# Optimization experiments

Measured on AMD Instinct MI355X. Metric: run time of the kernel, lower is better.

The kernel has to match this reference:

```python
import jax, jax.numpy as jnp
import numpy as np

BETA = 0.25  # commitment-loss weight


def setup_inputs() -> dict:
    key = jax.random.key(0)
    k1, k2 = jax.random.split(key)
    # x: [B, H, W, D] so that x.reshape(-1, D) groups per-pixel latent vectors
    x = jax.random.normal(k1, (32, 64, 64, 64), dtype=jnp.float32)
    # codebook: [D, K] as in the torch module (embedding_dim, num_embeddings)
    embedding = jax.random.normal(k2, (64, 1024), dtype=jnp.float32)
    return {"x": x, "embedding": embedding}


def reference(x, embedding):
    D, K = embedding.shape
    flat = x.reshape(-1, D)  # [N, D]
    # pairwise squared distances: ||z||^2 + ||e||^2 - 2 z.e  -> [N, K]
    distances = (
        jnp.sum(flat * flat, axis=1, keepdims=True)
        + jnp.sum(embedding * embedding, axis=0)
        - 2.0 * (flat @ embedding)
    )
    encoding_indices = jnp.argmin(distances, axis=1)  # [N]
    encodings = jax.nn.one_hot(encoding_indices, K, dtype=x.dtype)  # [N, K]
    # gather codewords (same math as encodings @ embedding.T, but O(N*D))
    quantized = jnp.take(embedding, encoding_indices, axis=1).T.reshape(x.shape)
    e_latent_loss = jnp.mean((jax.lax.stop_gradient(quantized) - x) ** 2)
    loss = BETA * e_latent_loss
    # straight-through estimator
    quantized_st = x + jax.lax.stop_gradient(quantized - x)
    avg_probs = jnp.mean(encodings, axis=0)
    perplexity = jnp.exp(-jnp.sum(avg_probs * jnp.log(avg_probs + 1e-10)))
    return quantized_st, loss, perplexity, encodings, encoding_indices
```

## Files before the change

### kernel.cpp

```cpp
#include <hip/hip_runtime.h>
#include <math.h>

#define NPIX    131072
#define DDIM    64
#define KCODE   1024
#define BETA    0.25f
#define EPS2    4e-3f
#define FIXCAP  2048
#define TAILROW 130944

#define Q_OFF    0
#define LOSS_OFF 8388608
#define PERP_OFF 8388609
#define ENC_OFF  8388610
#define IDX_OFF  142606338

#define TAIL_F     134086656
#define EHS_F      (TAIL_F + 2)
#define ELS_F      (TAIL_F + 32770)
#define FIXLIST_I  (TAIL_F + 65540)
#define FIXDELTA_F (TAIL_F + 69638)
#define FIXCOUNT_I (TAIL_F + 71688)


typedef _Float16 half8 __attribute__((ext_vector_type(8)));
typedef float    f32x4 __attribute__((ext_vector_type(4)));
typedef __attribute__((address_space(3))) void       lds_void_t;
typedef __attribute__((address_space(1))) const void g_void_t;

__global__ void vq_prep(const float* __restrict__ emb, float* __restrict__ embT,
                        _Float16* __restrict__ ehs, _Float16* __restrict__ els,
                        float* __restrict__ norms) {
    int b = blockIdx.x;
    if (b < 256) {
        int i = b * 256 + threadIdx.x;
        int d = i >> 10;
        int k = i & 1023;
        float v = emb[i];
        embT[k * DDIM + d] = v;
        _Float16 h = (_Float16)v;
        _Float16 l = (_Float16)(v - (float)h);
        int panel = k >> 6, codeP = k & 63;
        int sw = (d >> 3) ^ (k & 7);
        int fi = panel * 4096 + codeP * 64 + sw * 8 + (d & 7);
        ehs[fi] = h;
        els[fi] = l;
    } else {
        int k = (b - 256) * 256 + threadIdx.x;
        float s = 0.f;
        #pragma unroll 8
        for (int d = 0; d < DDIM; ++d) {
            float v = emb[d * KCODE + k];
            s = fmaf(v, v, s);
        }
        norms[k] = s;
    }
}

__global__ __launch_bounds__(256) void vq_fused(
        const float* __restrict__ x, const _Float16* __restrict__ ehs,
        const _Float16* __restrict__ els, const float* __restrict__ norms,
        const float* __restrict__ embT, float* __restrict__ idxf,
        float* __restrict__ q, float* __restrict__ enc,
        int* __restrict__ hist, float* __restrict__ lossp,
        int* __restrict__ fixlist, int* __restrict__ fixcount) {
    __shared__ __align__(16) char lds_raw[17152];

    const int tid  = threadIdx.x;
    const int role = blockIdx.x & 1;
    const int rid  = blockIdx.x >> 1;

    if (role == 1) {
        const long long NSEG = 33521663LL;
        f32x4* basep = (f32x4*)(enc + 2);
        f32x4 z = {0.f, 0.f, 0.f, 0.f};
        long long s = (long long)rid * 256 + tid;
        for (; s < NSEG; s += 262144LL) basep[s] = z;
        if (rid == 0 && tid == 0) {
            enc[0] = 0.f; enc[1] = 0.f;
            enc[TAIL_F - 2] = 0.f; enc[TAIL_F - 1] = 0.f;
        }
        return;
    }

    half8* EH8   = (half8*)lds_raw;
    half8* EL8   = (half8*)(lds_raw + 8192);
    float* NRM   = (float*)(lds_raw + 16384);
    int* idx_lds = (int*)(lds_raw + 16640);

    const int wave = tid >> 6;
    const int lane = tid & 63;
    const int lx = lane & 15;
    const int lk = lane >> 4;
    const int pixbase = rid * 128 + wave * 32;

    half8 ah[2][2], al[2][2];
    float xp0 = 0.f, xp1 = 0.f;
    #pragma unroll
    for (int mt = 0; mt < 2; ++mt) {
        const float* xr = x + (size_t)(pixbase + mt * 16 + lx) * DDIM + lk * 8;
        float xps = 0.f;
        #pragma unroll
        for (int kh = 0; kh < 2; ++kh) {
            float4 v0 = *(const float4*)(xr + kh * 32);
            float4 v1 = *(const float4*)(xr + kh * 32 + 4);
            xps = fmaf(v0.x, v0.x, xps); xps = fmaf(v0.y, v0.y, xps);
            xps = fmaf(v0.z, v0.z, xps); xps = fmaf(v0.w, v0.w, xps);
            xps = fmaf(v1.x, v1.x, xps); xps = fmaf(v1.y, v1.y, xps);
            xps = fmaf(v1.z, v1.z, xps); xps = fmaf(v1.w, v1.w, xps);
            half8 hh, ll;
            float vv;
            vv = v0.x; hh[0] = (_Float16)vv; ll[0] = (_Float16)(vv - (float)hh[0]);
            vv = v0.y; hh[1] = (_Float16)vv; ll[1] = (_Float16)(vv - (float)hh[1]);
            vv = v0.z; hh[2] = (_Float16)vv; ll[2] = (_Float16)(vv - (float)hh[2]);
            vv = v0.w; hh[3] = (_Float16)vv; ll[3] = (_Float16)(vv - (float)hh[3]);
            vv = v1.x; hh[4] = (_Float16)vv; ll[4] = (_Float16)(vv - (float)hh[4]);
            vv = v1.y; hh[5] = (_Float16)vv; ll[5] = (_Float16)(vv - (float)hh[5]);
            vv = v1.z; hh[6] = (_Float16)vv; ll[6] = (_Float16)(vv - (float)hh[6]);
            vv = v1.w; hh[7] = (_Float16)vv; ll[7] = (_Float16)(vv - (float)hh[7]);
            ah[mt][kh] = hh;
            al[mt][kh] = ll;
        }
        if (mt == 0) xp0 = xps; else xp1 = xps;
    }
    float xn0 = xp0 + __shfl_xor(xp0, 16); xn0 += __shfl_xor(xn0, 32);
    float xn1 = xp1 + __shfl_xor(xp1, 16); xn1 += __shfl_xor(xn1, 32);

    float b1[2][4], b2[2][4];
    int   i1[2][4];
    #pragma unroll
    for (int mt = 0; mt < 2; ++mt)
        #pragma unroll
        for (int r = 0; r < 4; ++r) { b1[mt][r] = 3.4e38f; b2[mt][r] = 3.4e38f; i1[mt][r] = 0; }

    #pragma unroll 1
    for (int t = 0; t < 16; ++t) {
        __syncthreads();
        {
            const char* gH = (const char*)ehs + (t << 13) + (tid << 4);
            const char* gL = (const char*)els + (t << 13) + (tid << 4);
            char* lH = &lds_raw[wave << 10];
            char* lL = &lds_raw[8192 + (wave << 10)];
            #pragma unroll
            for (int i = 0; i < 2; ++i) {
                __builtin_amdgcn_global_load_lds((g_void_t*)(gH + (i << 12)),
                                                 (lds_void_t*)(lH + (i << 12)), 16, 0, 0);
                __builtin_amdgcn_global_load_lds((g_void_t*)(gL + (i << 12)),
                                                 (lds_void_t*)(lL + (i << 12)), 16, 0, 0);
            }
            if (tid < 64) NRM[tid] = norms[t * 64 + tid];
        }
        __syncthreads();

        const int kbase = t * 64;
        #pragma unroll 1
        for (int c = 0; c < 4; ++c) {
            int code = c * 16 + lx;
            const half8* bhp = EH8 + code * 8;
            const half8* blp = EL8 + code * 8;
            int sw0 = lk ^ (code & 7);
            int sw1 = (lk + 4) ^ (code & 7);
            half8 bh0 = bhp[sw0], bh1 = bhp[sw1];
            half8 bl0 = blp[sw0], bl1 = blp[sw1];

            f32x4 acc0 = {0.f, 0.f, 0.f, 0.f};
            f32x4 acc1 = {0.f, 0.f, 0.f, 0.f};
            acc0 = __builtin_amdgcn_mfma_f32_16x16x32_f16(ah[0][0], bh0, acc0, 0, 0, 0);
            acc1 = __builtin_amdgcn_mfma_f32_16x16x32_f16(ah[1][0], bh0, acc1, 0, 0, 0);
            acc0 = __builtin_amdgcn_mfma_f32_16x16x32_f16(ah[0][1], bh1, acc0, 0, 0, 0);
            acc1 = __builtin_amdgcn_mfma_f32_16x16x32_f16(ah[1][1], bh1, acc1, 0, 0, 0);
            acc0 = __builtin_amdgcn_mfma_f32_16x16x32_f16(ah[0][0], bl0, acc0, 0, 0, 0);
            acc1 = __builtin_amdgcn_mfma_f32_16x16x32_f16(ah[1][0], bl0, acc1, 0, 0, 0);
            acc0 = __builtin_amdgcn_mfma_f32_16x16x32_f16(ah[0][1], bl1, acc0, 0, 0, 0);
            acc1 = __builtin_amdgcn_mfma_f32_16x16x32_f16(ah[1][1], bl1, acc1, 0, 0, 0);
            acc0 = __builtin_amdgcn_mfma_f32_16x16x32_f16(al[0][0], bh0, acc0, 0, 0, 0);
            acc1 = __builtin_amdgcn_mfma_f32_16x16x32_f16(al[1][0], bh0, acc1, 0, 0, 0);
            acc0 = __builtin_amdgcn_mfma_f32_16x16x32_f16(al[0][1], bh1, acc0, 0, 0, 0);
            acc1 = __builtin_amdgcn_mfma_f32_16x16x32_f16(al[1][1], bh1, acc1, 0, 0, 0);

            float nrm = NRM[c * 16 + lx];
            int codeg = kbase + c * 16 + lx;
            #pragma unroll
            for (int r = 0; r < 4; ++r) {
                float d0 = fmaf(-2.0f, acc0[r], nrm);
                bool lt0 = d0 < b1[0][r];
                b2[0][r] = fminf(b2[0][r], fmaxf(b1[0][r], d0));
                b1[0][r] = fminf(b1[0][r], d0);
                i1[0][r] = lt0 ? codeg : i1[0][r];
                float d1 = fmaf(-2.0f, acc1[r], nrm);
                bool lt1 = d1 < b1[1][r];
                b2[1][r] = fminf(b2[1][r], fmaxf(b1[1][r], d1));
                b1[1][r] = fminf(b1[1][r], d1);
                i1[1][r] = lt1 ? codeg : i1[1][r];
            }
        }
    }

    #pragma unroll
    for (int mt = 0; mt < 2; ++mt)
        #pragma unroll
        for (int r = 0; r < 4; ++r) {
            float a1 = b1[mt][r], a2 = b2[mt][r];
            int   ai = i1[mt][r];
            #pragma unroll
            for (int m = 1; m < 16; m <<= 1) {
                float c1 = __shfl_xor(a1, m, 64);
                float c2 = __shfl_xor(a2, m, 64);
                int   ci = __shfl_xor(ai, m, 64);
                if (c1 < a1 || (c1 == a1 && ci < ai)) {
                    a2 = fminf(a1, c2); a1 = c1; ai = ci;
                } else {
                    a2 = fminf(a2, c1);
                }
            }
            b1[mt][r] = a1; b2[mt][r] = a2; i1[mt][r] = ai;
        }

    float xfa[2][4];
    #pragma unroll
    for (int mt = 0; mt < 2; ++mt)
        #pragma unroll
        for (int r = 0; r < 4; ++r)
            xfa[mt][r] = __shfl(mt == 0 ? xn0 : xn1, lk * 4 + r, 64);

    if (lx == 0) {
        #pragma unroll
        for (int mt = 0; mt < 2; ++mt)
            #pragma unroll
            for (int r = 0; r < 4; ++r) {
                int p = mt * 16 + lk * 4 + r;
                int pixel = pixbase + p;
                idxf[pixel] = (float)i1[mt][r];
                idx_lds[wave * 32 + p] = i1[mt][r];
                atomicAdd(&hist[i1[mt][r]], 1);
                if (b2[mt][r] - b1[mt][r] < EPS2) {
                    int slot = atomicAdd(fixcount, 1);
                    if (slot < FIXCAP) {
                        fixlist[2 * slot]     = pixel;
                        fixlist[2 * slot + 1] = __float_as_int(b1[mt][r]);
                    }
                }
            }
    }

    float s8 = 0.f;
    #pragma unroll
    for (int mt = 0; mt < 2; ++mt)
        #pragma unroll
        for (int r = 0; r < 4; ++r) s8 += b1[mt][r] + xfa[mt][r];
    float sqv = (lx == 0) ? s8 : 0.f;
    #pragma unroll
    for (int m = 1; m < 64; m <<= 1) sqv += __shfl_xor(sqv, m, 64);
    if (lane == 0) lossp[rid * 4 + wave] = sqv;

    __syncthreads();
    const f32x4* eT4 = (const f32x4*)embT;
    f32x4* q4 = (f32x4*)q;
    #pragma unroll
    for (int it = 0; it < 8; ++it) {
        int i = it * 256 + tid;
        int r = i >> 4, j = i & 15;
        int idx = idx_lds[r];
        q4[((size_t)rid * 128 + r) * 16 + j] = eT4[idx * 16 + j];
    }
}

__global__ void vq_poke(const float* __restrict__ idxf, float* __restrict__ enc) {
    int n = blockIdx.x * 256 + threadIdx.x;
    if (n < TAILROW) {
        int idx = (int)idxf[n];
        enc[(size_t)n * 1024 + idx] = 1.f;
    }
}

__global__ __launch_bounds__(64) void vq_fixup(
        const float* __restrict__ x, const float* __restrict__ embT,
        const float* __restrict__ norms, const int* __restrict__ fixlist,
        const int* __restrict__ fixcount, float* __restrict__ idxf,
        float* __restrict__ q, float* __restrict__ enc,
        int* __restrict__ hist, float* __restrict__ fixdelta) {
    int cnt = *fixcount;
    if (cnt > FIXCAP) cnt = FIXCAP;
    int b = blockIdx.x;
    if (b >= cnt) return;
    int pixel = fixlist[2 * b];
    float b1old = __int_as_float(fixlist[2 * b + 1]);
    int lane = threadIdx.x;

    float xr[64];
    const float4* x4 = (const float4*)(x + (size_t)pixel * DDIM);
    #pragma unroll
    for (int j = 0; j < 16; ++j) {
        float4 v = x4[j];
        xr[j * 4] = v.x; xr[j * 4 + 1] = v.y; xr[j * 4 + 2] = v.z; xr[j * 4 + 3] = v.w;
    }
    float bd = 3.4e38f;
    int bi = 0;
    #pragma unroll 1
    for (int c = 0; c < 16; ++c) {
        int k = lane * 16 + c;
        const float4* e4 = (const float4*)(embT + (size_t)k * DDIM);
        float a0 = 0.f, a1 = 0.f, a2 = 0.f, a3 = 0.f;
        #pragma unroll
        for (int j = 0; j < 16; ++j) {
            float4 ev = e4[j];
            a0 = fmaf(xr[j * 4],     ev.x, a0);
            a1 = fmaf(xr[j * 4 + 1], ev.y, a1);
            a2 = fmaf(xr[j * 4 + 2], ev.z, a2);
            a3 = fmaf(xr[j * 4 + 3], ev.w, a3);
        }
        float dd = fmaf(-2.0f, (a0 + a1) + (a2 + a3), norms[k]);
        if (dd < bd) { bd = dd; bi = k; }
    }
    #pragma unroll
    for (int m = 1; m < 64; m <<= 1) {
        float od = __shfl_xor(bd, m, 64);
        int   oi = __shfl_xor(bi, m, 64);
        if (od < bd || (od == bd && oi < bi)) { bd = od; bi = oi; }
    }
    q[(size_t)pixel * DDIM + lane] = embT[(size_t)bi * DDIM + lane];
    if (lane == 0) {
        int old = (int)idxf[pixel];
        idxf[pixel] = (float)bi;
        fixdelta[b] = bd - b1old;
        if (bi != old) {
            atomicAdd(&hist[old], -1);
            atomicAdd(&hist[bi], 1);
            if (pixel < TAILROW) {
                enc[(size_t)pixel * 1024 + old] = 0.f;
                enc[(size_t)pixel * 1024 + bi]  = 1.f;
            }
        }
    }
}

__global__ void vq_final(const float* __restrict__ lossp, const int* __restrict__ hist,
                         const float* __restrict__ fixdelta,
                         const int* __restrict__ fixcount,
                         float* __restrict__ out_loss, float* __restrict__ out_perp) {
    __shared__ double red[256];
    int tid = threadIdx.x;
    double s = 0.0;
    for (int i = tid; i < 4096; i += 256) s += (double)lossp[i];
    red[tid] = s;
    __syncthreads();
    for (int st = 128; st > 0; st >>= 1) {
        if (tid < st) red[tid] += red[tid + st];
        __syncthreads();
    }
    if (tid == 0) {
        int cnt = *fixcount;
        if (cnt > FIXCAP) cnt = FIXCAP;
        double d = red[0];
        for (int i = 0; i < cnt; ++i) d += (double)fixdelta[i];
        *out_loss = (float)((double)BETA * d / (double)((size_t)NPIX * DDIM));
    }
    __syncthreads();

    double e = 0.0;
    for (int i = tid; i < KCODE; i += 256) {
        float p = (float)hist[i] / (float)NPIX;
        e += (double)(p * logf(p + 1e-10f));
    }
    red[tid] = e;
    __syncthreads();
    for (int st = 128; st > 0; st >>= 1) {
        if (tid < st) red[tid] += red[tid + st];
        __syncthreads();
    }
    if (tid == 0) *out_perp = expf((float)(-red[0]));
}

__global__ void vq_tail(const float* __restrict__ idxf, float* __restrict__ enc) {
    int r = blockIdx.x;
    int pixel = TAILROW + r;
    int idx = (int)idxf[pixel];
    size_t base = (size_t)pixel * 1024;
    int t = threadIdx.x;
    if (t < 255) {
        int k = 4 * t + 2;
        f32x4 v;
        v.x = (k     == idx) ? 1.f : 0.f;
        v.y = (k + 1 == idx) ? 1.f : 0.f;
        v.z = (k + 2 == idx) ? 1.f : 0.f;
        v.w = (k + 3 == idx) ? 1.f : 0.f;
        *(f32x4*)(enc + base + k) = v;
    } else {
        enc[base]        = (idx == 0)    ? 1.f : 0.f;
        enc[base + 1]    = (idx == 1)    ? 1.f : 0.f;
        enc[base + 1022] = (idx == 1022) ? 1.f : 0.f;
        enc[base + 1023] = (idx == 1023) ? 1.f : 0.f;
    }
}

extern "C" void kernel_launch(void* const* d_in, const int* in_sizes, int n_in,
                              void* d_out, int out_size, void* d_ws, size_t ws_size,
                              hipStream_t stream) {
    const float* x   = (const float*)d_in[0];
    const float* emb = (const float*)d_in[1];
    float* out = (float*)d_out;

    char* ws = (char*)d_ws;
    float* lossp = (float*)ws;
    int*   hist  = (int*)(ws + 32768);
    float* norms = (float*)(ws + 36864);
    float* embT  = (float*)(ws + 40960);

    float* q      = out + Q_OFF;
    float* o_loss = out + LOSS_OFF;
    float* o_perp = out + PERP_OFF;
    float* enc    = out + ENC_OFF;
    float* idxf   = out + IDX_OFF;

    _Float16* ehs   = (_Float16*)(enc + EHS_F);
    _Float16* els   = (_Float16*)(enc + ELS_F);
    int* fixlist    = (int*)(enc + FIXLIST_I);
    float* fixdelta = (float*)(enc + FIXDELTA_F);
    int* fixcount   = (int*)(enc + FIXCOUNT_I);

    (void)hipMemsetAsync(ws + 32768, 0, 4096, stream);
    (void)hipMemsetAsync((void*)fixcount, 0, 4, stream);

    vq_prep<<<260, 256, 0, stream>>>(emb, embT, ehs, els, norms);
    vq_fused<<<2048, 256, 0, stream>>>(x, ehs, els, norms, embT, idxf, q,
                                       enc, hist, lossp, fixlist, fixcount);
    vq_poke<<<512, 256, 0, stream>>>(idxf, enc);
    vq_fixup<<<FIXCAP, 64, 0, stream>>>(x, embT, norms, fixlist, fixcount,
                                        idxf, q, enc, hist, fixdelta);
    vq_final<<<1, 256, 0, stream>>>(lossp, hist, fixdelta, fixcount, o_loss, o_perp);
    vq_tail<<<128, 256, 0, stream>>>(idxf, enc);
}
```

Measured before the change: 244.3 us.

## Fuse one-hot zeroing and poke into argmin blocks with double-buffered codebook loads

Stops splitting blocks into separate zero-fill and compute roles. Each compute block now zeroes its own 128-row slice of the one-hot encodings, interleaved with a double-buffered async LDS prefetch of codebook tiles controlled by manual vmcnt waits, then writes its own one-hot ones, so the poke kernel is gone. Norms are loaded once into LDS, and the near-tie threshold for the fixup pass is tightened to send fewer pixels there. The aim is to hide the large zero-fill store traffic behind the MFMA distance work and remove a launch, at the cost of fragile hand-counted waitcnts and a narrower tie margin.

```diff
diff --git a/kernel.cpp b/kernel.cpp
--- a/kernel.cpp
+++ b/kernel.cpp
@@ -5,7 +5,7 @@
 #define DDIM    64
 #define KCODE   1024
 #define BETA    0.25f
-#define EPS2    4e-3f
+#define EPS2    1e-3f
 #define FIXCAP  2048
 #define TAILROW 130944
 
@@ -57,42 +57,27 @@
     }
 }
 
-__global__ __launch_bounds__(256) void vq_fused(
+__global__ __launch_bounds__(256) void vq_argmin_fused(
         const float* __restrict__ x, const _Float16* __restrict__ ehs,
         const _Float16* __restrict__ els, const float* __restrict__ norms,
         const float* __restrict__ embT, float* __restrict__ idxf,
         float* __restrict__ q, float* __restrict__ enc,
         int* __restrict__ hist, float* __restrict__ lossp,
         int* __restrict__ fixlist, int* __restrict__ fixcount) {
-    __shared__ __align__(16) char lds_raw[17152];
-
-    const int tid  = threadIdx.x;
-    const int role = blockIdx.x & 1;
-    const int rid  = blockIdx.x >> 1;
-
-    if (role == 1) {
-        const long long NSEG = 33521663LL;
-        f32x4* basep = (f32x4*)(enc + 2);
-        f32x4 z = {0.f, 0.f, 0.f, 0.f};
-        long long s = (long long)rid * 256 + tid;
-        for (; s < NSEG; s += 262144LL) basep[s] = z;
-        if (rid == 0 && tid == 0) {
-            enc[0] = 0.f; enc[1] = 0.f;
-            enc[TAIL_F - 2] = 0.f; enc[TAIL_F - 1] = 0.f;
-        }
-        return;
-    }
-
-    half8* EH8   = (half8*)lds_raw;
-    half8* EL8   = (half8*)(lds_raw + 8192);
-    float* NRM   = (float*)(lds_raw + 16384);
-    int* idx_lds = (int*)(lds_raw + 16640);
-
-    const int wave = tid >> 6;
-    const int lane = tid & 63;
+    __shared__ __align__(16) char lds_raw[37376];
+    float* NRMa  = (float*)(lds_raw + 32768);
+    int* idx_lds = (int*)(lds_raw + 36864);
+
+    const int tid   = threadIdx.x;
+    const int blkid = blockIdx.x;
+    const int wave  = tid >> 6;
+    const int lane  = tid & 63;
     const int lx = lane & 15;
     const int lk = lane >> 4;
-    const int pixbase = rid * 128 + wave * 32;
+    const int pixbase = blkid * 128 + wave * 32;
+
+    #pragma unroll
+    for (int i = 0; i < 4; ++i) NRMa[tid + i * 256] = norms[tid + i * 256];
 
     half8 ah[2][2], al[2][2];
     float xp0 = 0.f, xp1 = 0.f;
@@ -133,14 +118,36 @@
         #pragma unroll
         for (int r = 0; r < 4; ++r) { b1[mt][r] = 3.4e38f; b2[mt][r] = 3.4e38f; i1[mt][r] = 0; }
 
+    float* encB = enc + (size_t)blkid * 131072;
+    f32x4* zb = (f32x4*)(encB + 2);
+
+    __syncthreads();
+
+    {
+        const char* gH = (const char*)ehs + (tid << 4);
+        const char* gL = (const char*)els + (tid << 4);
+        char* lH = &lds_raw[(wave << 10)];
+        char* lL = &lds_raw[8192 + (wave << 10)];
+        #pragma unroll
+        for (int i = 0; i < 2; ++i) {
+            __builtin_amdgcn_global_load_lds((g_void_t*)(gH + (i << 12)),
+                                             (lds_void_t*)(lH + (i << 12)), 16, 0, 0);
+            __builtin_amdgcn_global_load_lds((g_void_t*)(gL + (i << 12)),
+                                             (lds_void_t*)(lL + (i << 12)), 16, 0, 0);
+        }
+    }
+
     #pragma unroll 1
     for (int t = 0; t < 16; ++t) {
-        __syncthreads();
-        {
-            const char* gH = (const char*)ehs + (t << 13) + (tid << 4);
-            const char* gL = (const char*)els + (t << 13) + (tid << 4);
-            char* lH = &lds_raw[wave << 10];
-            char* lL = &lds_raw[8192 + (wave << 10)];
+        __builtin_amdgcn_sched_barrier(0);
+        __builtin_amdgcn_s_barrier();
+        __builtin_amdgcn_sched_barrier(0);
+        if (t < 15) {
+            int nb = (t + 1) & 1;
+            const char* gH = (const char*)ehs + ((t + 1) << 13) + (tid << 4);
+            const char* gL = (const char*)els + ((t + 1) << 13) + (tid << 4);
+            char* lH = &lds_raw[(nb << 14) + (wave << 10)];
+            char* lL = &lds_raw[(nb << 14) + 8192 + (wave << 10)];
             #pragma unroll
             for (int i = 0; i < 2; ++i) {
                 __builtin_amdgcn_global_load_lds((g_void_t*)(gH + (i << 12)),
@@ -148,10 +155,29 @@
                 __builtin_amdgcn_global_load_lds((g_void_t*)(gL + (i << 12)),
                                                  (lds_void_t*)(lL + (i << 12)), 16, 0, 0);
             }
-            if (tid < 64) NRM[tid] = norms[t * 64 + tid];
-        }
-        __syncthreads();
-
+        }
+        __builtin_amdgcn_sched_barrier(0);
+        if (blkid != 1023) {
+            f32x4 z = {0.f, 0.f, 0.f, 0.f};
+            #pragma unroll
+            for (int it = 0; it < 8; ++it) {
+                int fi = t * 2048 + it * 256 + tid;
+                if (fi < 32767) zb[fi] = z;
+            }
+            __builtin_amdgcn_sched_barrier(0);
+            if (t == 0)       asm volatile("s_waitcnt vmcnt(12)" ::: "memory");
+            else if (t == 15) asm volatile("s_waitcnt vmcnt(16)" ::: "memory");
+            else              asm volatile("s_waitcnt vmcnt(20)" ::: "memory");
+        } else {
+            if (t == 15)      asm volatile("s_waitcnt vmcnt(0)" ::: "memory");
+            else              asm volatile("s_waitcnt vmcnt(4)" ::: "memory");
+        }
+        __builtin_amdgcn_sched_barrier(0);
+        __builtin_amdgcn_s_barrier();
+        __builtin_amdgcn_sched_barrier(0);
+
+        const half8* EH8 = (const half8*)(lds_raw + ((t & 1) << 14));
+        const half8* EL8 = (const half8*)(lds_raw + ((t & 1) << 14) + 8192);
         const int kbase = t * 64;
         #pragma unroll 1
         for (int c = 0; c < 4; ++c) {
@@ -178,7 +204,7 @@
             acc0 = __builtin_amdgcn_mfma_f32_16x16x32_f16(al[0][1], bh1, acc0, 0, 0, 0);
             acc1 = __builtin_amdgcn_mfma_f32_16x16x32_f16(al[1][1], bh1, acc1, 0, 0, 0);
 
-            float nrm = NRM[c * 16 + lx];
+            float nrm = NRMa[kbase + c * 16 + lx];
             int codeg = kbase + c * 16 + lx;
             #pragma unroll
             for (int r = 0; r < 4; ++r) {
@@ -194,7 +220,15 @@
                 i1[1][r] = lt1 ? codeg : i1[1][r];
             }
         }
-    }
+        __builtin_amdgcn_sched_barrier(0);
+    }
+
+    if (blkid != 1023 && tid == 0) {
+        encB[0] = 0.f; encB[1] = 0.f;
+        encB[131070] = 0.f; encB[131071] = 0.f;
+    }
+    asm volatile("s_waitcnt vmcnt(0)" ::: "memory");
+    __syncthreads();
 
     #pragma unroll
     for (int mt = 0; mt < 2; ++mt)
@@ -233,6 +267,8 @@
                 idxf[pixel] = (float)i1[mt][r];
                 idx_lds[wave * 32 + p] = i1[mt][r];
                 atomicAdd(&hist[i1[mt][r]], 1);
+                if (blkid != 1023)
+                    enc[(size_t)pixel * 1024 + i1[mt][r]] = 1.f;
                 if (b2[mt][r] - b1[mt][r] < EPS2) {
                     int slot = atomicAdd(fixcount, 1);
                     if (slot < FIXCAP) {
@@ -251,7 +287,7 @@
     float sqv = (lx == 0) ? s8 : 0.f;
     #pragma unroll
     for (int m = 1; m < 64; m <<= 1) sqv += __shfl_xor(sqv, m, 64);
-    if (lane == 0) lossp[rid * 4 + wave] = sqv;
+    if (lane == 0) lossp[blkid * 4 + wave] = sqv;
 
     __syncthreads();
     const f32x4* eT4 = (const f32x4*)embT;
@@ -261,15 +297,7 @@
         int i = it * 256 + tid;
         int r = i >> 4, j = i & 15;
         int idx = idx_lds[r];
-        q4[((size_t)rid * 128 + r) * 16 + j] = eT4[idx * 16 + j];
-    }
-}
-
-__global__ void vq_poke(const float* __restrict__ idxf, float* __restrict__ enc) {
-    int n = blockIdx.x * 256 + threadIdx.x;
-    if (n < TAILROW) {
-        int idx = (int)idxf[n];
-        enc[(size_t)n * 1024 + idx] = 1.f;
+        q4[((size_t)blkid * 128 + r) * 16 + j] = eT4[idx * 16 + j];
     }
 }
 
@@ -422,9 +450,8 @@
     (void)hipMemsetAsync((void*)fixcount, 0, 4, stream);
 
     vq_prep<<<260, 256, 0, stream>>>(emb, embT, ehs, els, norms);
-    vq_fused<<<2048, 256, 0, stream>>>(x, ehs, els, norms, embT, idxf, q,
-                                       enc, hist, lossp, fixlist, fixcount);
-    vq_poke<<<512, 256, 0, stream>>>(idxf, enc);
+    vq_argmin_fused<<<1024, 256, 0, stream>>>(x, ehs, els, norms, embT, idxf, q,
+                                              enc, hist, lossp, fixlist, fixcount);
     vq_fixup<<<FIXCAP, 64, 0, stream>>>(x, embT, norms, fixlist, fixcount,
                                         idxf, q, enc, hist, fixdelta);
     vq_final<<<1, 256, 0, stream>>>(lossp, hist, fixdelta, fixcount, o_loss, o_perp);
```

New measurement: 221.4 us. 9.3% less time.
